# Performance work log

Measured on AMD Instinct MI355X. Metric: run time of the kernel, lower is better.

The kernel has to match this reference:

```python
import jax, jax.numpy as jnp
import numpy as np

N, E, B = 100000, 1600000, 64
IN, HID, OUT, ED = 64, 128, 128, 2
K, ALPHA = 16, 0.1
LN_EPS = 1e-5


def setup_inputs() -> dict:
    key = jax.random.key(0)
    ks = jax.random.split(key, 24)
    def gl(k, shape, fan_in):
        return jax.random.uniform(k, shape, jnp.float32, -1.0, 1.0) / np.sqrt(fan_in)
    inp = {
        "x": jax.random.normal(ks[0], (N, IN), jnp.float32),
        "edge_index": jax.random.randint(ks[1], (2, E), 0, N, jnp.int64),
        "batch": jnp.sort(jax.random.randint(ks[2], (N,), 0, B, jnp.int64)),
        "edge_attr": jax.random.normal(ks[3], (E, ED), jnp.float32),
        # conv1: edge lin (ED->IN) + mlp (IN->HID->HID)
        "We1": gl(ks[4], (ED, IN), ED), "be1": jnp.zeros((IN,)),
        "W1a": gl(ks[5], (IN, HID), IN), "b1a": jnp.zeros((HID,)),
        "W1b": gl(ks[6], (HID, HID), HID), "b1b": jnp.zeros((HID,)),
        "g1": jnp.ones((HID,)), "bn1": jnp.zeros((HID,)),
        # conv2: edge lin (ED->HID) + mlp (HID->OUT->OUT)
        "We2": gl(ks[7], (ED, HID), ED), "be2": jnp.zeros((HID,)),
        "W2a": gl(ks[8], (HID, OUT), HID), "b2a": jnp.zeros((OUT,)),
        "W2b": gl(ks[9], (OUT, OUT), OUT), "b2b": jnp.zeros((OUT,)),
        "g2": jnp.ones((OUT,)), "bn2": jnp.zeros((OUT,)),
        # gate nn (OUT -> OUT//2 -> 1)
        "Wg1": gl(ks[10], (OUT, OUT // 2), OUT), "bg1": jnp.zeros((OUT // 2,)),
        "Wg2": gl(ks[11], (OUT // 2, 1), OUT // 2), "bg2": jnp.zeros((1,)),
    }
    return inp


def _gelu(x):
    return jax.nn.gelu(x, approximate=False)


def _layernorm(x, g, b):
    mu = jnp.mean(x, axis=-1, keepdims=True)
    var = jnp.mean(jnp.square(x - mu), axis=-1, keepdims=True)
    return (x - mu) * jax.lax.rsqrt(var + LN_EPS) * g + b


def _gine(x, src, dst, edge_attr, We, be, W1, b1, W2, b2):
    # message: ReLU(x_j + lin(edge_attr)), aggregated by sum at dst; eps=0
    m = jax.nn.relu(x[src] + edge_attr @ We + be)          # [E, d]
    agg = jax.ops.segment_sum(m, dst, num_segments=N)      # [N, d]
    h = x + agg
    return _gelu(h @ W1 + b1) @ W2 + b2


def _appnp(x, src, dst):
    # gcn_norm with self-loops: deg_i = 1 + in-degree
    deg = jax.ops.segment_sum(jnp.ones((E,), x.dtype), dst, num_segments=N) + 1.0
    dis = jax.lax.rsqrt(deg)
    w = dis[src] * dis[dst]            # [E]
    selfw = 1.0 / deg                  # [N]
    def step(i, h):
        prop = jax.ops.segment_sum(w[:, None] * h[src], dst, num_segments=N) \
               + selfw[:, None] * h
        return (1.0 - ALPHA) * prop + ALPHA * x
    return jax.lax.fori_loop(0, K, step, x)


def reference(x, edge_index, batch, edge_attr,
              We1, be1, W1a, b1a, W1b, b1b, g1, bn1,
              We2, be2, W2a, b2a, W2b, b2b, g2, bn2,
              Wg1, bg1, Wg2, bg2):
    src, dst = edge_index[0], edge_index[1]
    h = _gine(x, src, dst, edge_attr, We1, be1, W1a, b1a, W1b, b1b)
    h = _layernorm(_gelu(h), g1, bn1)
    # dropout is identity in eval
    h = _gine(h, src, dst, edge_attr, We2, be2, W2a, b2a, W2b, b2b)
    h = _layernorm(h, g2, bn2)
    h = _appnp(h, src, dst)
    # attentional aggregation: per-graph softmax over gate scores
    gate = (_gelu(h @ Wg1 + bg1) @ Wg2 + bg2)[:, 0]        # [N]
    m = jax.ops.segment_max(gate, batch, num_segments=B)    # [B]
    e = jnp.exp(gate - m[batch])
    s = jax.ops.segment_sum(e, batch, num_segments=B)
    a = e / s[batch]
    g = jax.ops.segment_sum(a[:, None] * h, batch, num_segments=B)  # [B, OUT]
    return h, g
```

## Files before the change

### kernel.cpp

```cpp
#include <hip/hip_runtime.h>
#include <math.h>

#define N_NODES 100000
#define N_EDGES 1600000
#define N_B 64
#define D_IN 64
#define D_HID 128
#define D_OUT 128
#define K_ITER 16
#define LN_EPS 1e-5f

typedef short s8v __attribute__((ext_vector_type(8)));
typedef float f4v __attribute__((ext_vector_type(4)));

__device__ __forceinline__ float gelu_f(float x) {
    return 0.5f * x * (1.0f + erff(0.70710678118654752440f * x));
}

__device__ __forceinline__ unsigned pack_bf2(float a, float b) {
    unsigned ua = __float_as_uint(a), ub = __float_as_uint(b);
    ua += 0x7fffu + ((ua >> 16) & 1u);
    ub += 0x7fffu + ((ub >> 16) & 1u);
    return (ua >> 16) | (ub & 0xffff0000u);
}
__device__ __forceinline__ float ubx(unsigned u) { return __uint_as_float(u << 16); }
__device__ __forceinline__ float uby(unsigned u) { return __uint_as_float(u & 0xffff0000u); }

__device__ __forceinline__ unsigned short bf_rne(float x) {
    unsigned u = __float_as_uint(x);
    u += 0x7fffu + ((u >> 16) & 1u);
    return (unsigned short)(u >> 16);
}
__device__ __forceinline__ float bf_f(unsigned short s) {
    return __uint_as_float(((unsigned)s) << 16);
}


__global__ __launch_bounds__(256) void hist_kernel(const int* __restrict__ dst, int* __restrict__ counts) {
    int e = blockIdx.x * 256 + threadIdx.x;
    if (e < N_EDGES) atomicAdd(&counts[dst[e]], 1);
}

__global__ __launch_bounds__(256) void deg_kernel(const int* __restrict__ counts,
                                                  float* __restrict__ dis, float* __restrict__ selfw) {
    int i = blockIdx.x * 256 + threadIdx.x;
    if (i < N_NODES) {
        float d = (float)(counts[i] + 1);
        dis[i] = 1.0f / sqrtf(d);
        selfw[i] = 1.0f / d;
    }
}

__global__ __launch_bounds__(1024) void scan1(const int* __restrict__ counts, int* __restrict__ rp,
                                              int* __restrict__ bsum) {
    __shared__ int tmp[1024];
    int t = threadIdx.x;
    int idx = blockIdx.x * 1024 + t;
    int v = (idx < N_NODES) ? counts[idx] : 0;
    tmp[t] = v;
    __syncthreads();
    for (int o = 1; o < 1024; o <<= 1) {
        int add = (t >= o) ? tmp[t - o] : 0;
        __syncthreads();
        tmp[t] += add;
        __syncthreads();
    }
    if (idx < N_NODES) rp[idx] = tmp[t] - v;
    if (t == 1023) bsum[blockIdx.x] = tmp[t];
}

__global__ void scan2(int* bsum, int nb) {
    if (threadIdx.x == 0 && blockIdx.x == 0) {
        int acc = 0;
        for (int i = 0; i < nb; i++) { int v = bsum[i]; bsum[i] = acc; acc += v; }
    }
}

__global__ __launch_bounds__(1024) void scan3(int* __restrict__ rp, const int* __restrict__ bsum,
                                              int* __restrict__ cursor) {
    int t = threadIdx.x;
    int idx = blockIdx.x * 1024 + t;
    if (idx < N_NODES) {
        int v = rp[idx] + bsum[blockIdx.x];
        rp[idx] = v;
        cursor[idx] = v;
    }
    if (idx == 0) rp[N_NODES] = N_EDGES;
}

__global__ __launch_bounds__(256) void scatter_kernel(const int* __restrict__ src, const int* __restrict__ dst,
                                                      const float* __restrict__ ea, const float* __restrict__ dis,
                                                      int* __restrict__ cursor, int2* __restrict__ esw,
                                                      float2* __restrict__ eea) {
    int e = blockIdx.x * 256 + threadIdx.x;
    if (e >= N_EDGES) return;
    int s = src[e], d = dst[e];
    int pos = atomicAdd(&cursor[d], 1);
    int2 sw;
    sw.x = s;
    sw.y = __float_as_int(dis[s] * dis[d]);
    esw[pos] = sw;
    float2 e2;
    e2.x = ea[e * 2];
    e2.y = ea[e * 2 + 1];
    eea[pos] = e2;
}


__global__ __launch_bounds__(256) void conv1_gather(const float* __restrict__ x, const int* __restrict__ rp,
                                                    const int2* __restrict__ esw, const float2* __restrict__ eea,
                                                    const float* __restrict__ We1, const float* __restrict__ be1,
                                                    float* __restrict__ out) {
    int gw = (blockIdx.x * 256 + threadIdx.x) >> 6;
    if (gw >= N_NODES) return;
    int lane = threadIdx.x & 63;
    float w0 = We1[lane], w1 = We1[64 + lane], bb = be1[lane];
    float acc = x[(size_t)gw * 64 + lane];
    int j = rp[gw], s1 = rp[gw + 1];
    for (; j + 4 <= s1; j += 4) {
        int2 e0 = esw[j], e1 = esw[j + 1], e2 = esw[j + 2], e3 = esw[j + 3];
        float2 a0 = eea[j], a1 = eea[j + 1], a2 = eea[j + 2], a3 = eea[j + 3];
        float v0 = x[(size_t)e0.x * 64 + lane];
        float v1 = x[(size_t)e1.x * 64 + lane];
        float v2 = x[(size_t)e2.x * 64 + lane];
        float v3 = x[(size_t)e3.x * 64 + lane];
        acc += fmaxf(v0 + a0.x * w0 + a0.y * w1 + bb, 0.0f);
        acc += fmaxf(v1 + a1.x * w0 + a1.y * w1 + bb, 0.0f);
        acc += fmaxf(v2 + a2.x * w0 + a2.y * w1 + bb, 0.0f);
        acc += fmaxf(v3 + a3.x * w0 + a3.y * w1 + bb, 0.0f);
    }
    for (; j < s1; j++) {
        int2 e = esw[j];
        float2 a = eea[j];
        float v = x[(size_t)e.x * 64 + lane];
        acc += fmaxf(v + a.x * w0 + a.y * w1 + bb, 0.0f);
    }
    out[(size_t)gw * 64 + lane] = acc;
}

__global__ __launch_bounds__(256) void conv2_gather(const float* __restrict__ h1, const int* __restrict__ rp,
                                                    const int2* __restrict__ esw, const float2* __restrict__ eea,
                                                    const float* __restrict__ We2, const float* __restrict__ be2,
                                                    float* __restrict__ out) {
    int gw = (blockIdx.x * 256 + threadIdx.x) >> 6;
    if (gw >= N_NODES) return;
    int lane = threadIdx.x & 63;
    int f0 = lane * 2;
    float w00 = We2[f0], w01 = We2[f0 + 1];
    float w10 = We2[128 + f0], w11 = We2[128 + f0 + 1];
    float b0 = be2[f0], b1 = be2[f0 + 1];
    const float2* h2 = (const float2*)h1;
    float2 hc = h2[(size_t)gw * 64 + lane];
    float a0 = hc.x, a1 = hc.y;
    int j = rp[gw], s1 = rp[gw + 1];
    for (; j + 8 <= s1; j += 8) {
        int2 e0 = esw[j], e1 = esw[j + 1], e2 = esw[j + 2], e3 = esw[j + 3];
        int2 e4 = esw[j + 4], e5 = esw[j + 5], e6 = esw[j + 6], e7 = esw[j + 7];
        float2 q0 = eea[j], q1 = eea[j + 1], q2 = eea[j + 2], q3 = eea[j + 3];
        float2 q4 = eea[j + 4], q5 = eea[j + 5], q6 = eea[j + 6], q7 = eea[j + 7];
        float2 v0 = h2[(size_t)e0.x * 64 + lane];
        float2 v1 = h2[(size_t)e1.x * 64 + lane];
        float2 v2 = h2[(size_t)e2.x * 64 + lane];
        float2 v3 = h2[(size_t)e3.x * 64 + lane];
        float2 v4 = h2[(size_t)e4.x * 64 + lane];
        float2 v5 = h2[(size_t)e5.x * 64 + lane];
        float2 v6 = h2[(size_t)e6.x * 64 + lane];
        float2 v7 = h2[(size_t)e7.x * 64 + lane];
        a0 += fmaxf(v0.x + q0.x * w00 + q0.y * w10 + b0, 0.0f);
        a1 += fmaxf(v0.y + q0.x * w01 + q0.y * w11 + b1, 0.0f);
        a0 += fmaxf(v1.x + q1.x * w00 + q1.y * w10 + b0, 0.0f);
        a1 += fmaxf(v1.y + q1.x * w01 + q1.y * w11 + b1, 0.0f);
        a0 += fmaxf(v2.x + q2.x * w00 + q2.y * w10 + b0, 0.0f);
        a1 += fmaxf(v2.y + q2.x * w01 + q2.y * w11 + b1, 0.0f);
        a0 += fmaxf(v3.x + q3.x * w00 + q3.y * w10 + b0, 0.0f);
        a1 += fmaxf(v3.y + q3.x * w01 + q3.y * w11 + b1, 0.0f);
        a0 += fmaxf(v4.x + q4.x * w00 + q4.y * w10 + b0, 0.0f);
        a1 += fmaxf(v4.y + q4.x * w01 + q4.y * w11 + b1, 0.0f);
        a0 += fmaxf(v5.x + q5.x * w00 + q5.y * w10 + b0, 0.0f);
        a1 += fmaxf(v5.y + q5.x * w01 + q5.y * w11 + b1, 0.0f);
        a0 += fmaxf(v6.x + q6.x * w00 + q6.y * w10 + b0, 0.0f);
        a1 += fmaxf(v6.y + q6.x * w01 + q6.y * w11 + b1, 0.0f);
        a0 += fmaxf(v7.x + q7.x * w00 + q7.y * w10 + b0, 0.0f);
        a1 += fmaxf(v7.y + q7.x * w01 + q7.y * w11 + b1, 0.0f);
    }
    for (; j < s1; j++) {
        int2 e = esw[j];
        float2 q = eea[j];
        float2 v = h2[(size_t)e.x * 64 + lane];
        a0 += fmaxf(v.x + q.x * w00 + q.y * w10 + b0, 0.0f);
        a1 += fmaxf(v.y + q.x * w01 + q.y * w11 + b1, 0.0f);
    }
    out[(size_t)gw * 128 + f0] = a0;
    out[(size_t)gw * 128 + f0 + 1] = a1;
}


template <int Kd, bool GELU, bool LN>
__global__ __launch_bounds__(256) void mlp_mfma(const float* __restrict__ A, const float* __restrict__ W,
                                                const float* __restrict__ bias, const float* __restrict__ g,
                                                const float* __restrict__ bn, float* __restrict__ out) {
    __shared__ unsigned short sHi[8192];
    __shared__ unsigned short sLo[8192];
    int wave = threadIdx.x >> 6, lane = threadIdx.x & 63;
    int quad = lane >> 4, n = lane & 15;
    int rowA = blockIdx.x * 64 + wave * 16 + n;
    int rowAc = (rowA < N_NODES) ? rowA : 0;

    f4v acc[8];
    #pragma unroll
    for (int t = 0; t < 8; t++) acc[t] = (f4v){0.f, 0.f, 0.f, 0.f};

    for (int ph = 0; ph < Kd / 64; ph++) {
        __syncthreads();
        for (int idx = threadIdx.x; idx < 8192; idx += 256) {
            int k = idx >> 7, c = idx & 127;
            float v = W[(size_t)(ph * 64 + k) * 128 + c];
            unsigned short hi = bf_rne(v);
            unsigned short lo = bf_rne(v - bf_f(hi));
            int kk = k >> 5, q = (k >> 3) & 3, j = k & 7, t = c >> 4, nn = c & 15;
            int lidx = ((((kk * 4 + q) * 8 + t) * 16 + nn) << 3) + j;
            sHi[lidx] = hi;
            sLo[lidx] = lo;
        }
        __syncthreads();
        #pragma unroll
        for (int kk = 0; kk < 2; kk++) {
            int k0 = ph * 64 + kk * 32 + quad * 8;
            const float4* ap = (const float4*)(A + (size_t)rowAc * Kd + k0);
            float4 a0 = ap[0], a1 = ap[1];
            float av[8] = {a0.x, a0.y, a0.z, a0.w, a1.x, a1.y, a1.z, a1.w};
            s8v ahi, alo;
            #pragma unroll
            for (int j = 0; j < 8; j++) {
                unsigned short h = bf_rne(av[j]);
                ahi[j] = (short)h;
                alo[j] = (short)bf_rne(av[j] - bf_f(h));
            }
            int base = ((kk * 4 + quad) * 8) * 128;
            #pragma unroll
            for (int t = 0; t < 8; t++) {
                s8v bhi = *(const s8v*)&sHi[base + ((t * 16 + n) << 3)];
                s8v blo = *(const s8v*)&sLo[base + ((t * 16 + n) << 3)];
                acc[t] = __builtin_amdgcn_mfma_f32_16x16x32_bf16(ahi, bhi, acc[t], 0, 0, 0);
                acc[t] = __builtin_amdgcn_mfma_f32_16x16x32_bf16(ahi, blo, acc[t], 0, 0, 0);
                acc[t] = __builtin_amdgcn_mfma_f32_16x16x32_bf16(alo, bhi, acc[t], 0, 0, 0);
            }
        }
    }

    float bcol[8], gcol[8], bncol[8];
    #pragma unroll
    for (int t = 0; t < 8; t++) {
        bcol[t] = bias[t * 16 + n];
        if (LN) { gcol[t] = g[t * 16 + n]; bncol[t] = bn[t * 16 + n]; }
    }
    #pragma unroll
    for (int r = 0; r < 4; r++) {
        int row = blockIdx.x * 64 + wave * 16 + quad * 4 + r;
        float v[8];
        #pragma unroll
        for (int t = 0; t < 8; t++) {
            float x = acc[t][r] + bcol[t];
            v[t] = GELU ? gelu_f(x) : x;
        }
        if (LN) {
            float s = 0.f, q2 = 0.f;
            #pragma unroll
            for (int t = 0; t < 8; t++) { s += v[t]; q2 += v[t] * v[t]; }
            #pragma unroll
            for (int m = 1; m <= 8; m <<= 1) {
                s += __shfl_xor(s, m, 64);
                q2 += __shfl_xor(q2, m, 64);
            }
            float mu = s * (1.0f / 128.0f);
            float rs = rsqrtf(q2 * (1.0f / 128.0f) - mu * mu + LN_EPS);
            #pragma unroll
            for (int t = 0; t < 8; t++) v[t] = (v[t] - mu) * rs * gcol[t] + bncol[t];
        }
        if (row < N_NODES) {
            #pragma unroll
            for (int t = 0; t < 8; t++) out[(size_t)row * 128 + t * 16 + n] = v[t];
        }
    }
}


__global__ __launch_bounds__(256) void gate_mfma(const float* __restrict__ h, const float* __restrict__ Wg1,
                                                 const float* __restrict__ bg1, const float* __restrict__ Wg2,
                                                 const float* __restrict__ bg2, float* __restrict__ gate) {
    __shared__ unsigned short sHi[8192];
    __shared__ unsigned short sLo[8192];
    int wave = threadIdx.x >> 6, lane = threadIdx.x & 63;
    int quad = lane >> 4, n = lane & 15;
    for (int idx = threadIdx.x; idx < 8192; idx += 256) {
        int k = idx >> 6, c = idx & 63;
        float v = Wg1[k * 64 + c];
        unsigned short hi = bf_rne(v);
        unsigned short lo = bf_rne(v - bf_f(hi));
        int kk = k >> 5, q = (k >> 3) & 3, j = k & 7, t = c >> 4, nn = c & 15;
        int lidx = ((((kk * 4 + q) * 4 + t) * 16 + nn) << 3) + j;
        sHi[lidx] = hi;
        sLo[lidx] = lo;
    }
    __syncthreads();
    int rowA = blockIdx.x * 64 + wave * 16 + n;
    int rowAc = (rowA < N_NODES) ? rowA : 0;
    f4v acc[4];
    #pragma unroll
    for (int t = 0; t < 4; t++) acc[t] = (f4v){0.f, 0.f, 0.f, 0.f};
    #pragma unroll
    for (int kk = 0; kk < 4; kk++) {
        const float4* ap = (const float4*)(h + (size_t)rowAc * 128 + kk * 32 + quad * 8);
        float4 a0 = ap[0], a1 = ap[1];
        float av[8] = {a0.x, a0.y, a0.z, a0.w, a1.x, a1.y, a1.z, a1.w};
        s8v ahi, alo;
        #pragma unroll
        for (int j = 0; j < 8; j++) {
            unsigned short hh = bf_rne(av[j]);
            ahi[j] = (short)hh;
            alo[j] = (short)bf_rne(av[j] - bf_f(hh));
        }
        int base = ((kk * 4 + quad) * 4) * 128;
        #pragma unroll
        for (int t = 0; t < 4; t++) {
            s8v bhi = *(const s8v*)&sHi[base + ((t * 16 + n) << 3)];
            s8v blo = *(const s8v*)&sLo[base + ((t * 16 + n) << 3)];
            acc[t] = __builtin_amdgcn_mfma_f32_16x16x32_bf16(ahi, bhi, acc[t], 0, 0, 0);
            acc[t] = __builtin_amdgcn_mfma_f32_16x16x32_bf16(ahi, blo, acc[t], 0, 0, 0);
            acc[t] = __builtin_amdgcn_mfma_f32_16x16x32_bf16(alo, bhi, acc[t], 0, 0, 0);
        }
    }
    float b2 = bg2[0];
    float bb[4], vv[4];
    #pragma unroll
    for (int t = 0; t < 4; t++) { bb[t] = bg1[t * 16 + n]; vv[t] = Wg2[t * 16 + n]; }
    #pragma unroll
    for (int r = 0; r < 4; r++) {
        int row = blockIdx.x * 64 + wave * 16 + quad * 4 + r;
        float val = 0.f;
        #pragma unroll
        for (int t = 0; t < 4; t++) val += gelu_f(acc[t][r] + bb[t]) * vv[t];
        #pragma unroll
        for (int m = 1; m <= 8; m <<= 1) val += __shfl_xor(val, m, 64);
        if (n == 0 && row < N_NODES) gate[row] = val + b2;
    }
}


__global__ __launch_bounds__(256) void f32_to_bf2(const float2* __restrict__ in, unsigned* __restrict__ out) {
    int i = blockIdx.x * 256 + threadIdx.x;
    if (i < N_NODES * 64) { float2 v = in[i]; out[i] = pack_bf2(v.x, v.y); }
}

template <bool LAST>
__global__ __launch_bounds__(256) void appnp_step_bf(const unsigned* __restrict__ hin,
                                                     const float2* __restrict__ anchor,
                                                     unsigned* __restrict__ hout, float2* __restrict__ houtf,
                                                     const int* __restrict__ rp, const int2* __restrict__ esw,
                                                     const float* __restrict__ selfw) {
    int gw = (blockIdx.x * 256 + threadIdx.x) >> 6;
    if (gw >= N_NODES) return;
    int lane = threadIdx.x & 63;
    size_t idx = (size_t)gw * 64 + lane;
    float swi = selfw[gw];
    unsigned hcp = hin[idx];
    float ax = swi * ubx(hcp), ay = swi * uby(hcp);
    int j = rp[gw], s1 = rp[gw + 1];
    for (; j + 8 <= s1; j += 8) {
        int2 e0 = esw[j], e1 = esw[j + 1], e2 = esw[j + 2], e3 = esw[j + 3];
        int2 e4 = esw[j + 4], e5 = esw[j + 5], e6 = esw[j + 6], e7 = esw[j + 7];
        unsigned v0 = hin[(size_t)e0.x * 64 + lane];
        unsigned v1 = hin[(size_t)e1.x * 64 + lane];
        unsigned v2 = hin[(size_t)e2.x * 64 + lane];
        unsigned v3 = hin[(size_t)e3.x * 64 + lane];
        unsigned v4 = hin[(size_t)e4.x * 64 + lane];
        unsigned v5 = hin[(size_t)e5.x * 64 + lane];
        unsigned v6 = hin[(size_t)e6.x * 64 + lane];
        unsigned v7 = hin[(size_t)e7.x * 64 + lane];
        float w0 = __int_as_float(e0.y), w1 = __int_as_float(e1.y);
        float w2 = __int_as_float(e2.y), w3 = __int_as_float(e3.y);
        float w4 = __int_as_float(e4.y), w5 = __int_as_float(e5.y);
        float w6 = __int_as_float(e6.y), w7 = __int_as_float(e7.y);
        ax = fmaf(w0, ubx(v0), ax); ay = fmaf(w0, uby(v0), ay);
        ax = fmaf(w1, ubx(v1), ax); ay = fmaf(w1, uby(v1), ay);
        ax = fmaf(w2, ubx(v2), ax); ay = fmaf(w2, uby(v2), ay);
        ax = fmaf(w3, ubx(v3), ax); ay = fmaf(w3, uby(v3), ay);
        ax = fmaf(w4, ubx(v4), ax); ay = fmaf(w4, uby(v4), ay);
        ax = fmaf(w5, ubx(v5), ax); ay = fmaf(w5, uby(v5), ay);
        ax = fmaf(w6, ubx(v6), ax); ay = fmaf(w6, uby(v6), ay);
        ax = fmaf(w7, ubx(v7), ax); ay = fmaf(w7, uby(v7), ay);
    }
    for (; j + 4 <= s1; j += 4) {
        int2 e0 = esw[j], e1 = esw[j + 1], e2 = esw[j + 2], e3 = esw[j + 3];
        unsigned v0 = hin[(size_t)e0.x * 64 + lane];
        unsigned v1 = hin[(size_t)e1.x * 64 + lane];
        unsigned v2 = hin[(size_t)e2.x * 64 + lane];
        unsigned v3 = hin[(size_t)e3.x * 64 + lane];
        float w0 = __int_as_float(e0.y), w1 = __int_as_float(e1.y);
        float w2 = __int_as_float(e2.y), w3 = __int_as_float(e3.y);
        ax = fmaf(w0, ubx(v0), ax); ay = fmaf(w0, uby(v0), ay);
        ax = fmaf(w1, ubx(v1), ax); ay = fmaf(w1, uby(v1), ay);
        ax = fmaf(w2, ubx(v2), ax); ay = fmaf(w2, uby(v2), ay);
        ax = fmaf(w3, ubx(v3), ax); ay = fmaf(w3, uby(v3), ay);
    }
    for (; j < s1; j++) {
        int2 e = esw[j];
        unsigned v = hin[(size_t)e.x * 64 + lane];
        float w = __int_as_float(e.y);
        ax = fmaf(w, ubx(v), ax); ay = fmaf(w, uby(v), ay);
    }
    float2 anc = anchor[idx];
    float ox = 0.9f * ax + 0.1f * anc.x;
    float oy = 0.9f * ay + 0.1f * anc.y;
    if (LAST) {
        float2 o; o.x = ox; o.y = oy;
        houtf[idx] = o;
    } else {
        hout[idx] = pack_bf2(ox, oy);
    }
}


__global__ void seg_begin(const int* __restrict__ batch, int* __restrict__ gbeg) {
    int b = threadIdx.x;
    if (b > N_B) return;
    if (b == N_B) { gbeg[N_B] = N_NODES; return; }
    int lo = 0, hi = N_NODES;
    while (lo < hi) {
        int mid = (lo + hi) >> 1;
        if (batch[mid] < b) lo = mid + 1; else hi = mid;
    }
    gbeg[b] = lo;
}

__global__ __launch_bounds__(256) void seg_max(const float* __restrict__ gate, const int* __restrict__ gbeg,
                                               float* __restrict__ gmax) {
    int b = blockIdx.x;
    int s = gbeg[b], e = gbeg[b + 1];
    float m = -INFINITY;
    for (int i = s + threadIdx.x; i < e; i += 256) m = fmaxf(m, gate[i]);
    for (int o = 32; o > 0; o >>= 1) m = fmaxf(m, __shfl_xor(m, o, 64));
    __shared__ float red[4];
    if ((threadIdx.x & 63) == 0) red[threadIdx.x >> 6] = m;
    __syncthreads();
    if (threadIdx.x == 0) gmax[b] = fmaxf(fmaxf(red[0], red[1]), fmaxf(red[2], red[3]));
}

__global__ __launch_bounds__(256) void seg_sum(const float* __restrict__ gate, const int* __restrict__ gbeg,
                                               const float* __restrict__ gmax, float* __restrict__ gsum) {
    int b = blockIdx.x;
    int s = gbeg[b], e = gbeg[b + 1];
    float m = gmax[b];
    float acc = 0.0f;
    for (int i = s + threadIdx.x; i < e; i += 256) acc += expf(gate[i] - m);
    for (int o = 32; o > 0; o >>= 1) acc += __shfl_xor(acc, o, 64);
    __shared__ float red[4];
    if ((threadIdx.x & 63) == 0) red[threadIdx.x >> 6] = acc;
    __syncthreads();
    if (threadIdx.x == 0) gsum[b] = red[0] + red[1] + red[2] + red[3];
}

__global__ __launch_bounds__(512) void seg_pool(const float* __restrict__ h, const float* __restrict__ gate,
                                                const int* __restrict__ gbeg, const float* __restrict__ gmax,
                                                const float* __restrict__ gsum, float* __restrict__ gout) {
    int b = blockIdx.x >> 3, slice = blockIdx.x & 7;
    int team = threadIdx.x >> 7;
    int f = threadIdx.x & 127;
    int s = gbeg[b], e = gbeg[b + 1];
    float m = gmax[b];
    float inv = (e > s) ? 1.0f / gsum[b] : 0.0f;
    float acc = 0.0f;
    for (int i = s + slice * 4 + team; i < e; i += 32) {
        float a = expf(gate[i] - m) * inv;
        acc = fmaf(a, h[(size_t)i * 128 + f], acc);
    }
    __shared__ float red[4][128];
    red[team][f] = acc;
    __syncthreads();
    if (team == 0) {
        float v = red[0][f] + red[1][f] + red[2][f] + red[3][f];
        atomicAdd(&gout[b * 128 + f], v);
    }
}


extern "C" void kernel_launch(void* const* d_in, const int* in_sizes, int n_in,
                              void* d_out, int out_size, void* d_ws, size_t ws_size,
                              hipStream_t stream) {
    const float* x     = (const float*)d_in[0];
    const int*   ei    = (const int*)d_in[1];
    const int*   batch = (const int*)d_in[2];
    const float* ea    = (const float*)d_in[3];
    const float* We1 = (const float*)d_in[4];
    const float* be1 = (const float*)d_in[5];
    const float* W1a = (const float*)d_in[6];
    const float* b1a = (const float*)d_in[7];
    const float* W1b = (const float*)d_in[8];
    const float* b1b = (const float*)d_in[9];
    const float* g1  = (const float*)d_in[10];
    const float* bn1 = (const float*)d_in[11];
    const float* We2 = (const float*)d_in[12];
    const float* be2 = (const float*)d_in[13];
    const float* W2a = (const float*)d_in[14];
    const float* b2a = (const float*)d_in[15];
    const float* W2b = (const float*)d_in[16];
    const float* b2b = (const float*)d_in[17];
    const float* g2  = (const float*)d_in[18];
    const float* bn2 = (const float*)d_in[19];
    const float* Wg1 = (const float*)d_in[20];
    const float* bg1 = (const float*)d_in[21];
    const float* Wg2 = (const float*)d_in[22];
    const float* bg2 = (const float*)d_in[23];

    float* outH = (float*)d_out;
    float* outG = outH + (size_t)N_NODES * 128;

    char* w = (char*)d_ws;
    auto carve = [&](size_t bytes) {
        void* p = (void*)w;
        w += ((bytes + 255) / 256) * 256;
        return p;
    };
    float*  bufB   = (float*)carve((size_t)N_NODES * 128 * 4);
    float*  bufC   = (float*)carve((size_t)N_NODES * 128 * 4);
    int2*   esw    = (int2*)carve((size_t)N_EDGES * 8);
    float2* eea    = (float2*)carve((size_t)N_EDGES * 8);
    int*    counts = (int*)carve((size_t)N_NODES * 4);
    int*    rp     = (int*)carve((size_t)(N_NODES + 1) * 4);
    int*    cursor = (int*)carve((size_t)N_NODES * 4);
    float*  dis    = (float*)carve((size_t)N_NODES * 4);
    float*  selfw  = (float*)carve((size_t)N_NODES * 4);
    float*  gate   = (float*)carve((size_t)N_NODES * 4);
    int*    bsum   = (int*)carve(128 * 4);
    float*  gmax   = (float*)carve(N_B * 4);
    float*  gsum   = (float*)carve(N_B * 4);
    int*    gbeg   = (int*)carve((N_B + 1) * 4);

    const int* src = ei;
    const int* dst = ei + N_EDGES;

    const int NB_SCAN = (N_NODES + 1023) / 1024;
    const int EB = (N_EDGES + 255) / 256;
    const int NBLK = (N_NODES + 255) / 256;
    const int WBLK = (N_NODES + 3) / 4;
    const int MBLK = (N_NODES + 63) / 64;

    hipMemsetAsync(counts, 0, (size_t)N_NODES * 4, stream);
    hist_kernel<<<EB, 256, 0, stream>>>(dst, counts);
    deg_kernel<<<NBLK, 256, 0, stream>>>(counts, dis, selfw);
    scan1<<<NB_SCAN, 1024, 0, stream>>>(counts, rp, bsum);
    scan2<<<1, 64, 0, stream>>>(bsum, NB_SCAN);
    scan3<<<NB_SCAN, 1024, 0, stream>>>(rp, bsum, cursor);
    scatter_kernel<<<EB, 256, 0, stream>>>(src, dst, ea, dis, cursor, esw, eea);

    conv1_gather<<<WBLK, 256, 0, stream>>>(x, rp, esw, eea, We1, be1, bufB);
    mlp_mfma<64, true, false><<<MBLK, 256, 0, stream>>>(bufB, W1a, b1a, nullptr, nullptr, outH);
    mlp_mfma<128, true, true><<<MBLK, 256, 0, stream>>>(outH, W1b, b1b, g1, bn1, bufB);

    conv2_gather<<<WBLK, 256, 0, stream>>>(bufB, rp, esw, eea, We2, be2, bufC);
    mlp_mfma<128, true, false><<<MBLK, 256, 0, stream>>>(bufC, W2a, b2a, nullptr, nullptr, outH);
    mlp_mfma<128, false, true><<<MBLK, 256, 0, stream>>>(outH, W2b, b2b, g2, bn2, bufB);

    unsigned* bfA = (unsigned*)bufC;
    unsigned* bfB2 = bfA + (size_t)N_NODES * 64;
    const float2* anchor2 = (const float2*)bufB;
    f32_to_bf2<<<(N_NODES * 64 + 255) / 256, 256, 0, stream>>>(anchor2, bfA);
    const unsigned* cur = bfA;
    for (int k = 1; k <= K_ITER - 1; k++) {
        unsigned* dstbuf = (k & 1) ? bfB2 : bfA;
        appnp_step_bf<false><<<WBLK, 256, 0, stream>>>(cur, anchor2, dstbuf, nullptr, rp, esw, selfw);
        cur = dstbuf;
    }
    appnp_step_bf<true><<<WBLK, 256, 0, stream>>>(cur, anchor2, nullptr, (float2*)outH, rp, esw, selfw);

    gate_mfma<<<MBLK, 256, 0, stream>>>(outH, Wg1, bg1, Wg2, bg2, gate);
    seg_begin<<<1, 128, 0, stream>>>(batch, gbeg);
    seg_max<<<N_B, 256, 0, stream>>>(gate, gbeg, gmax);
    seg_sum<<<N_B, 256, 0, stream>>>(gate, gbeg, gmax, gsum);
    hipMemsetAsync(outG, 0, (size_t)N_B * 128 * 4, stream);
    seg_pool<<<N_B * 8, 512, 0, stream>>>(outH, gate, gbeg, gmax, gsum, outG);
}
```

Measured before the change: 1.981 ms.

## Emit bf16 copies from MLP epilogues for conv2 gather and APPNP anchor

The MLP epilogues gain an output mode that writes bf16 copies, alongside or instead of the fp32 result. conv2 then gathers neighbor features in bf16 instead of fp32, which halves the gather bytes. The standalone f32-to-bf16 conversion kernel is removed because the last MLP writes the bf16 anchor directly, and APPNP reads that bf16 anchor. The trade-off is lower precision in the conv2 messages and in the APPNP anchor term, plus a bf16 write in the layer-1 epilogue.

After: 1.834 ms. -7.4%, faster.

```diff
diff --git a/kernel.cpp b/kernel.cpp
--- a/kernel.cpp
+++ b/kernel.cpp
@@ -17,12 +17,6 @@
     return 0.5f * x * (1.0f + erff(0.70710678118654752440f * x));
 }
 
-__device__ __forceinline__ unsigned pack_bf2(float a, float b) {
-    unsigned ua = __float_as_uint(a), ub = __float_as_uint(b);
-    ua += 0x7fffu + ((ua >> 16) & 1u);
-    ub += 0x7fffu + ((ub >> 16) & 1u);
-    return (ua >> 16) | (ub & 0xffff0000u);
-}
 __device__ __forceinline__ float ubx(unsigned u) { return __uint_as_float(u << 16); }
 __device__ __forceinline__ float uby(unsigned u) { return __uint_as_float(u & 0xffff0000u); }
 
@@ -33,6 +27,9 @@
 }
 __device__ __forceinline__ float bf_f(unsigned short s) {
     return __uint_as_float(((unsigned)s) << 16);
+}
+__device__ __forceinline__ unsigned pack_bf2(float a, float b) {
+    return (unsigned)bf_rne(a) | (((unsigned)bf_rne(b)) << 16);
 }
 
 
@@ -138,7 +135,8 @@
     out[(size_t)gw * 64 + lane] = acc;
 }
 
-__global__ __launch_bounds__(256) void conv2_gather(const float* __restrict__ h1, const int* __restrict__ rp,
+__global__ __launch_bounds__(256) void conv2_gather(const float* __restrict__ h1f, const unsigned* __restrict__ h1b,
+                                                    const int* __restrict__ rp,
                                                     const int2* __restrict__ esw, const float2* __restrict__ eea,
                                                     const float* __restrict__ We2, const float* __restrict__ be2,
                                                     float* __restrict__ out) {
@@ -149,8 +147,7 @@
     float w00 = We2[f0], w01 = We2[f0 + 1];
     float w10 = We2[128 + f0], w11 = We2[128 + f0 + 1];
     float b0 = be2[f0], b1 = be2[f0 + 1];
-    const float2* h2 = (const float2*)h1;
-    float2 hc = h2[(size_t)gw * 64 + lane];
+    float2 hc = ((const float2*)h1f)[(size_t)gw * 64 + lane];
     float a0 = hc.x, a1 = hc.y;
     int j = rp[gw], s1 = rp[gw + 1];
     for (; j + 8 <= s1; j += 8) {
@@ -158,47 +155,48 @@
         int2 e4 = esw[j + 4], e5 = esw[j + 5], e6 = esw[j + 6], e7 = esw[j + 7];
         float2 q0 = eea[j], q1 = eea[j + 1], q2 = eea[j + 2], q3 = eea[j + 3];
         float2 q4 = eea[j + 4], q5 = eea[j + 5], q6 = eea[j + 6], q7 = eea[j + 7];
-        float2 v0 = h2[(size_t)e0.x * 64 + lane];
-        float2 v1 = h2[(size_t)e1.x * 64 + lane];
-        float2 v2 = h2[(size_t)e2.x * 64 + lane];
-        float2 v3 = h2[(size_t)e3.x * 64 + lane];
-        float2 v4 = h2[(size_t)e4.x * 64 + lane];
-        float2 v5 = h2[(size_t)e5.x * 64 + lane];
-        float2 v6 = h2[(size_t)e6.x * 64 + lane];
-        float2 v7 = h2[(size_t)e7.x * 64 + lane];
-        a0 += fmaxf(v0.x + q0.x * w00 + q0.y * w10 + b0, 0.0f);
-        a1 += fmaxf(v0.y + q0.x * w01 + q0.y * w11 + b1, 0.0f);
-        a0 += fmaxf(v1.x + q1.x * w00 + q1.y * w10 + b0, 0.0f);
-        a1 += fmaxf(v1.y + q1.x * w01 + q1.y * w11 + b1, 0.0f);
-        a0 += fmaxf(v2.x + q2.x * w00 + q2.y * w10 + b0, 0.0f);
-        a1 += fmaxf(v2.y + q2.x * w01 + q2.y * w11 + b1, 0.0f);
-        a0 += fmaxf(v3.x + q3.x * w00 + q3.y * w10 + b0, 0.0f);
-        a1 += fmaxf(v3.y + q3.x * w01 + q3.y * w11 + b1, 0.0f);
-        a0 += fmaxf(v4.x + q4.x * w00 + q4.y * w10 + b0, 0.0f);
-        a1 += fmaxf(v4.y + q4.x * w01 + q4.y * w11 + b1, 0.0f);
-        a0 += fmaxf(v5.x + q5.x * w00 + q5.y * w10 + b0, 0.0f);
-        a1 += fmaxf(v5.y + q5.x * w01 + q5.y * w11 + b1, 0.0f);
-        a0 += fmaxf(v6.x + q6.x * w00 + q6.y * w10 + b0, 0.0f);
-        a1 += fmaxf(v6.y + q6.x * w01 + q6.y * w11 + b1, 0.0f);
-        a0 += fmaxf(v7.x + q7.x * w00 + q7.y * w10 + b0, 0.0f);
-        a1 += fmaxf(v7.y + q7.x * w01 + q7.y * w11 + b1, 0.0f);
+        unsigned v0 = h1b[(size_t)e0.x * 64 + lane];
+        unsigned v1 = h1b[(size_t)e1.x * 64 + lane];
+        unsigned v2 = h1b[(size_t)e2.x * 64 + lane];
+        unsigned v3 = h1b[(size_t)e3.x * 64 + lane];
+        unsigned v4 = h1b[(size_t)e4.x * 64 + lane];
+        unsigned v5 = h1b[(size_t)e5.x * 64 + lane];
+        unsigned v6 = h1b[(size_t)e6.x * 64 + lane];
+        unsigned v7 = h1b[(size_t)e7.x * 64 + lane];
+        a0 += fmaxf(ubx(v0) + q0.x * w00 + q0.y * w10 + b0, 0.0f);
+        a1 += fmaxf(uby(v0) + q0.x * w01 + q0.y * w11 + b1, 0.0f);
+        a0 += fmaxf(ubx(v1) + q1.x * w00 + q1.y * w10 + b0, 0.0f);
+        a1 += fmaxf(uby(v1) + q1.x * w01 + q1.y * w11 + b1, 0.0f);
+        a0 += fmaxf(ubx(v2) + q2.x * w00 + q2.y * w10 + b0, 0.0f);
+        a1 += fmaxf(uby(v2) + q2.x * w01 + q2.y * w11 + b1, 0.0f);
+        a0 += fmaxf(ubx(v3) + q3.x * w00 + q3.y * w10 + b0, 0.0f);
+        a1 += fmaxf(uby(v3) + q3.x * w01 + q3.y * w11 + b1, 0.0f);
+        a0 += fmaxf(ubx(v4) + q4.x * w00 + q4.y * w10 + b0, 0.0f);
+        a1 += fmaxf(uby(v4) + q4.x * w01 + q4.y * w11 + b1, 0.0f);
+        a0 += fmaxf(ubx(v5) + q5.x * w00 + q5.y * w10 + b0, 0.0f);
+        a1 += fmaxf(uby(v5) + q5.x * w01 + q5.y * w11 + b1, 0.0f);
+        a0 += fmaxf(ubx(v6) + q6.x * w00 + q6.y * w10 + b0, 0.0f);
+        a1 += fmaxf(uby(v6) + q6.x * w01 + q6.y * w11 + b1, 0.0f);
+        a0 += fmaxf(ubx(v7) + q7.x * w00 + q7.y * w10 + b0, 0.0f);
+        a1 += fmaxf(uby(v7) + q7.x * w01 + q7.y * w11 + b1, 0.0f);
     }
     for (; j < s1; j++) {
         int2 e = esw[j];
         float2 q = eea[j];
-        float2 v = h2[(size_t)e.x * 64 + lane];
-        a0 += fmaxf(v.x + q.x * w00 + q.y * w10 + b0, 0.0f);
-        a1 += fmaxf(v.y + q.x * w01 + q.y * w11 + b1, 0.0f);
+        unsigned v = h1b[(size_t)e.x * 64 + lane];
+        a0 += fmaxf(ubx(v) + q.x * w00 + q.y * w10 + b0, 0.0f);
+        a1 += fmaxf(uby(v) + q.x * w01 + q.y * w11 + b1, 0.0f);
     }
     out[(size_t)gw * 128 + f0] = a0;
     out[(size_t)gw * 128 + f0 + 1] = a1;
 }
 
 
-template <int Kd, bool GELU, bool LN>
+template <int Kd, bool GELU, bool LN, int OMODE>
 __global__ __launch_bounds__(256) void mlp_mfma(const float* __restrict__ A, const float* __restrict__ W,
                                                 const float* __restrict__ bias, const float* __restrict__ g,
-                                                const float* __restrict__ bn, float* __restrict__ out) {
+                                                const float* __restrict__ bn, float* __restrict__ outf,
+                                                unsigned short* __restrict__ outb) {
     __shared__ unsigned short sHi[8192];
     __shared__ unsigned short sLo[8192];
     int wave = threadIdx.x >> 6, lane = threadIdx.x & 63;
@@ -279,7 +277,10 @@
         }
         if (row < N_NODES) {
             #pragma unroll
-            for (int t = 0; t < 8; t++) out[(size_t)row * 128 + t * 16 + n] = v[t];
+            for (int t = 0; t < 8; t++) {
+                if (OMODE != 2) outf[(size_t)row * 128 + t * 16 + n] = v[t];
+                if (OMODE >= 1) outb[(size_t)row * 128 + t * 16 + n] = bf_rne(v[t]);
+            }
         }
     }
 }
@@ -347,14 +348,9 @@
 }
 
 
-__global__ __launch_bounds__(256) void f32_to_bf2(const float2* __restrict__ in, unsigned* __restrict__ out) {
-    int i = blockIdx.x * 256 + threadIdx.x;
-    if (i < N_NODES * 64) { float2 v = in[i]; out[i] = pack_bf2(v.x, v.y); }
-}
-
 template <bool LAST>
 __global__ __launch_bounds__(256) void appnp_step_bf(const unsigned* __restrict__ hin,
-                                                     const float2* __restrict__ anchor,
+                                                     const unsigned* __restrict__ anchor,
                                                      unsigned* __restrict__ hout, float2* __restrict__ houtf,
                                                      const int* __restrict__ rp, const int2* __restrict__ esw,
                                                      const float* __restrict__ selfw) {
@@ -409,9 +405,9 @@
         float w = __int_as_float(e.y);
         ax = fmaf(w, ubx(v), ax); ay = fmaf(w, uby(v), ay);
     }
-    float2 anc = anchor[idx];
-    float ox = 0.9f * ax + 0.1f * anc.x;
-    float oy = 0.9f * ay + 0.1f * anc.y;
+    unsigned ancp = anchor[idx];
+    float ox = 0.9f * ax + 0.1f * ubx(ancp);
+    float oy = 0.9f * ay + 0.1f * uby(ancp);
     if (LAST) {
         float2 o; o.x = ox; o.y = oy;
         houtf[idx] = o;
@@ -553,25 +549,26 @@
     scan3<<<NB_SCAN, 1024, 0, stream>>>(rp, bsum, cursor);
     scatter_kernel<<<EB, 256, 0, stream>>>(src, dst, ea, dis, cursor, esw, eea);
 
+    unsigned short* h1bf  = (unsigned short*)bufC;
+    unsigned* ancU  = (unsigned*)bufC;
+    unsigned* pingA = ancU + (size_t)N_NODES * 64;
+    unsigned* pingB = (unsigned*)bufB;
+
     conv1_gather<<<WBLK, 256, 0, stream>>>(x, rp, esw, eea, We1, be1, bufB);
-    mlp_mfma<64, true, false><<<MBLK, 256, 0, stream>>>(bufB, W1a, b1a, nullptr, nullptr, outH);
-    mlp_mfma<128, true, true><<<MBLK, 256, 0, stream>>>(outH, W1b, b1b, g1, bn1, bufB);
-
-    conv2_gather<<<WBLK, 256, 0, stream>>>(bufB, rp, esw, eea, We2, be2, bufC);
-    mlp_mfma<128, true, false><<<MBLK, 256, 0, stream>>>(bufC, W2a, b2a, nullptr, nullptr, outH);
-    mlp_mfma<128, false, true><<<MBLK, 256, 0, stream>>>(outH, W2b, b2b, g2, bn2, bufB);
-
-    unsigned* bfA = (unsigned*)bufC;
-    unsigned* bfB2 = bfA + (size_t)N_NODES * 64;
-    const float2* anchor2 = (const float2*)bufB;
-    f32_to_bf2<<<(N_NODES * 64 + 255) / 256, 256, 0, stream>>>(anchor2, bfA);
-    const unsigned* cur = bfA;
+    mlp_mfma<64, true, false, 0><<<MBLK, 256, 0, stream>>>(bufB, W1a, b1a, nullptr, nullptr, outH, nullptr);
+    mlp_mfma<128, true, true, 1><<<MBLK, 256, 0, stream>>>(outH, W1b, b1b, g1, bn1, bufB, h1bf);
+
+    conv2_gather<<<WBLK, 256, 0, stream>>>(bufB, (const unsigned*)h1bf, rp, esw, eea, We2, be2, outH);
+    mlp_mfma<128, true, false, 0><<<MBLK, 256, 0, stream>>>(outH, W2a, b2a, nullptr, nullptr, bufB, nullptr);
+    mlp_mfma<128, false, true, 2><<<MBLK, 256, 0, stream>>>(bufB, W2b, b2b, g2, bn2, nullptr, (unsigned short*)ancU);
+
+    const unsigned* cur = ancU;
     for (int k = 1; k <= K_ITER - 1; k++) {
-        unsigned* dstbuf = (k & 1) ? bfB2 : bfA;
-        appnp_step_bf<false><<<WBLK, 256, 0, stream>>>(cur, anchor2, dstbuf, nullptr, rp, esw, selfw);
+        unsigned* dstbuf = (k & 1) ? pingA : pingB;
+        appnp_step_bf<false><<<WBLK, 256, 0, stream>>>(cur, ancU, dstbuf, nullptr, rp, esw, selfw);
         cur = dstbuf;
     }
-    appnp_step_bf<true><<<WBLK, 256, 0, stream>>>(cur, anchor2, nullptr, (float2*)outH, rp, esw, selfw);
+    appnp_step_bf<true><<<WBLK, 256, 0, stream>>>(cur, ancU, nullptr, (float2*)outH, rp, esw, selfw);
 
     gate_mfma<<<MBLK, 256, 0, stream>>>(outH, Wg1, bg1, Wg2, bg2, gate);
     seg_begin<<<1, 128, 0, stream>>>(batch, gbeg);
```
